# Performance work log

Hardware: AMD Instinct MI355X
Metric: run time of the kernel (lower is better)

Reference implementation:

```python
import jax, jax.numpy as jnp
import numpy as np

N_NODES = 100000


def setup_inputs() -> dict:
    key = jax.random.key(0)
    k1, k2, k3, k4, k5 = jax.random.split(key, 5)
    in_f, out_f, E = 128, 128, 1600000
    std = 1.0 / np.sqrt(out_f)
    H = jax.random.normal(k1, (N_NODES, in_f), dtype=jnp.float32)
    W = jax.random.uniform(k2, (in_f, out_f), minval=-std, maxval=std, dtype=jnp.float32)
    bias = jax.random.uniform(k3, (out_f,), minval=-std, maxval=std, dtype=jnp.float32)
    row = jax.random.randint(k4, (E,), 0, N_NODES, dtype=jnp.int32)
    col = jax.random.randint(k5, (E,), 0, N_NODES, dtype=jnp.int32)
    return {"H": H, "W": W, "bias": bias, "row": row, "col": col}


def reference(H, W, bias, row, col):
    # H: [N, in_f]; W: [in_f, out_f]; row/col: [E] edge endpoints
    Hp = jnp.matmul(H, W)  # [N, out_f]
    # edge-wise attention: leaky_relu(<Hp[i], Hp[j]>)
    scores = jax.nn.leaky_relu(jnp.sum(Hp[row] * Hp[col], axis=-1), negative_slope=0.2)  # [E]
    # scatter-softmax over rows (matches sparse_softmax: exp / (row_sum + 1e-10))
    ex = jnp.exp(scores)
    denom = jax.ops.segment_sum(ex, row, num_segments=N_NODES)  # [N]
    attn = ex / (denom[row] + 1e-10)  # [E]
    # sparse-matmul aggregation: out[i] = sum_e attn[e] * Hp[col[e]]
    out = jax.ops.segment_sum(attn[:, None] * Hp[col], row, num_segments=N_NODES)  # [N, out_f]
    return out + bias
```

## Files before the change

kernel.cpp:

```cpp
#include <hip/hip_runtime.h>
#include <hip/hip_bf16.h>

#define RSH 7
#define RPB (1 << RSH)
#define CSH 17
#define CMASK ((1 << CSH) - 1)
#define CHUNK_E 8192
#define CAP 4096
#define NBMAX 1024

typedef __attribute__((ext_vector_type(8))) _Float16 f16x8;
typedef __attribute__((ext_vector_type(2))) _Float16 f16x2;
typedef __attribute__((ext_vector_type(4))) float f32x4;

__device__ __forceinline__ unsigned int pack2h(float a, float b) {
    union { _Float16 h[2]; unsigned int u; } c;
    c.h[0] = (_Float16)a; c.h[1] = (_Float16)b;
    return c.u;
}
__device__ __forceinline__ unsigned short f2h_bits(float f) {
    union { _Float16 h; unsigned short u; } c;
    c.h = (_Float16)f;
    return c.u;
}

__global__ __launch_bounds__(256) void wsplit(
    const float* __restrict__ Wg, unsigned int* __restrict__ WhiG)
{
    int task = blockIdx.x * 256 + threadIdx.x;
    if (task >= 2048) return;
    int n  = task & 127;
    int k0 = (task >> 7) * 8;
    unsigned int hi[4];
    #pragma unroll
    for (int j = 0; j < 4; ++j) {
        float w0 = Wg[(size_t)(k0 + 2*j)     * 128 + n];
        float w1 = Wg[(size_t)(k0 + 2*j + 1) * 128 + n];
        hi[j] = pack2h(w0, w1);
    }
    int byte = (k0 * 2) ^ ((n & 7) << 4);
    *(uint4*)((char*)WhiG + n * 256 + byte) = make_uint4(hi[0], hi[1], hi[2], hi[3]);
}

__global__ __launch_bounds__(512) void gemm_hist(
    const float* __restrict__ H, const unsigned int* __restrict__ WhiG,
    unsigned short* __restrict__ Hpb, int N,
    const int* __restrict__ row, unsigned short* __restrict__ Ht,
    int E, int nchunk, int nb2, int gemmBlocks)
{
    __shared__ unsigned short Ahi[128 * 128];
    __shared__ unsigned short Whi[128 * 128];
    const int tid = threadIdx.x;

    if (blockIdx.x >= gemmBlocks) {
        int* cnt = (int*)Ahi;
        const int c = blockIdx.x - gemmBlocks;
        for (int i = tid; i < nb2; i += 512) cnt[i] = 0;
        __syncthreads();
        const int e0 = c * CHUNK_E;
        const int e1 = min(e0 + CHUNK_E, E);
        for (int e = e0 + tid; e < e1; e += 512)
            atomicAdd(&cnt[row[e] >> RSH], 1);
        __syncthreads();
        for (int i = tid; i < nb2; i += 512)
            Ht[(size_t)i * nchunk + c] = (unsigned short)cnt[i];
        return;
    }

    const int rbase = blockIdx.x * 128;

    #pragma unroll
    for (int i = 0; i < 4; ++i) {
        int idx = tid + 512 * i;
        ((uint4*)Whi)[idx] = ((const uint4*)WhiG)[idx];
    }
    #pragma unroll
    for (int i = 0; i < 8; ++i) {
        int flat = tid + 512 * i;
        int rr = flat >> 5;
        int c4  = (flat & 31) * 4;
        float4 h = make_float4(0.f, 0.f, 0.f, 0.f);
        if (rbase + rr < N)
            h = *(const float4*)&H[(size_t)(rbase + rr) * 128 + c4];
        uint2 vh;
        vh.x = pack2h(h.x, h.y);
        vh.y = pack2h(h.z, h.w);
        int byte = (c4 * 2) ^ ((rr & 7) << 4);
        *(uint2*)((char*)Ahi + rr * 256 + byte) = vh;
    }
    __syncthreads();

    const int wid = tid >> 6, lane = tid & 63;
    const int wm = wid >> 1, wn = wid & 1;
    const int lr = lane & 15, lg = lane >> 4;
    f32x4 acc[2][4] = {};

    #pragma unroll
    for (int ks = 0; ks < 4; ++ks) {
        const int kb = ks * 64 + lg * 16;
        f16x8 ahi[2];
        #pragma unroll
        for (int mi = 0; mi < 2; ++mi) {
            int rr = wm * 32 + mi * 16 + lr;
            int sw = kb ^ ((rr & 7) << 4);
            ahi[mi] = *(const f16x8*)((char*)Ahi + rr * 256 + sw);
        }
        #pragma unroll
        for (int nf = 0; nf < 4; ++nf) {
            int n = wn * 64 + nf * 16 + lr;
            int sw = kb ^ ((n & 7) << 4);
            f16x8 bhi = *(const f16x8*)((char*)Whi + n * 256 + sw);
            #pragma unroll
            for (int mi = 0; mi < 2; ++mi)
                acc[mi][nf] = __builtin_amdgcn_mfma_f32_16x16x32_f16(ahi[mi], bhi, acc[mi][nf], 0, 0, 0);
        }
    }

    #pragma unroll
    for (int mi = 0; mi < 2; ++mi) {
        #pragma unroll
        for (int nf = 0; nf < 4; ++nf) {
            int col = wn * 64 + nf * 16 + lr;
            #pragma unroll
            for (int i = 0; i < 4; ++i) {
                int rr = rbase + wm * 32 + mi * 16 + lg * 4 + i;
                if (rr < N)
                    Hpb[(size_t)rr * 128 + col] = f2h_bits(acc[mi][nf][i]);
            }
        }
    }
}

__global__ __launch_bounds__(256) void bucket_scan(
    const unsigned short* __restrict__ Ht, unsigned short* __restrict__ rel,
    int* __restrict__ totals, int nchunk)
{
    __shared__ int s[256];
    const int b = blockIdx.x, tid = threadIdx.x;
    int v = (tid < nchunk) ? (int)Ht[(size_t)b * nchunk + tid] : 0;
    s[tid] = v;
    __syncthreads();
    for (int d = 1; d < 256; d <<= 1) {
        int t = (tid >= d) ? s[tid - d] : 0;
        __syncthreads();
        s[tid] += t;
        __syncthreads();
    }
    if (tid < nchunk) rel[(size_t)b * nchunk + tid] = (unsigned short)(s[tid] - v);
    if (tid == 255) totals[b] = s[255];
}

__global__ __launch_bounds__(1024) void bucket_ptr_scan(
    const int* __restrict__ totals, int* __restrict__ bucketptr, int nb2)
{
    __shared__ int s[1024];
    const int tid = threadIdx.x;
    int v = (tid < nb2) ? totals[tid] : 0;
    s[tid] = v;
    __syncthreads();
    for (int d = 1; d < 1024; d <<= 1) {
        int t = (tid >= d) ? s[tid - d] : 0;
        __syncthreads();
        s[tid] += t;
        __syncthreads();
    }
    if (tid < nb2) bucketptr[tid] = s[tid] - v;
    if (tid == nb2 - 1) bucketptr[nb2] = s[tid];
}

__global__ __launch_bounds__(256) void chunk_scatter(
    const int* __restrict__ row, const int* __restrict__ col,
    const unsigned short* __restrict__ rel, const int* __restrict__ bucketptr,
    int* __restrict__ colsort, int E, int nchunk, int nb2)
{
    __shared__ int cur[NBMAX];
    __shared__ int gb[NBMAX];
    const int tid = threadIdx.x;
    const int c = blockIdx.x;
    const int e0 = c * CHUNK_E;
    const int tot = min(CHUNK_E, E - e0);

    for (int b = tid; b < nb2; b += 256) {
        cur[b] = 0;
        gb[b] = bucketptr[b] + (int)rel[(size_t)b * nchunk + c];
    }
    __syncthreads();

    for (int j = tid; j < tot; j += 256) {
        int r = row[e0 + j], cc = col[e0 + j];
        int b = r >> RSH;
        int p = atomicAdd(&cur[b], 1);
        colsort[gb[b] + p] = ((r & (RPB - 1)) << CSH) | cc;
    }
}

__global__ __launch_bounds__(256) void bucket_sort(
    const int* __restrict__ bucketptr, int* __restrict__ rowptr,
    int* __restrict__ colsort, int N)
{
    __shared__ int rcnt[RPB];
    __shared__ int rcur[RPB];
    __shared__ int sc[256];
    __shared__ int ord[CAP];
    const int b = blockIdx.x, tid = threadIdx.x;
    const int rbase = b << RSH;
    const int s0 = bucketptr[b];
    const int cnt = bucketptr[b + 1] - s0;

    if (tid < RPB) rcnt[tid] = 0;
    __syncthreads();
    for (int j = tid; j < cnt; j += 256)
        atomicAdd(&rcnt[colsort[s0 + j] >> CSH], 1);
    __syncthreads();

    int v = (tid < RPB) ? rcnt[tid] : 0;
    sc[tid] = v;
    __syncthreads();
    for (int d = 1; d < RPB; d <<= 1) {
        int t = (tid >= d) ? sc[tid - d] : 0;
        __syncthreads();
        sc[tid] += t;
        __syncthreads();
    }
    if (tid < RPB) {
        int ex = sc[tid] - v;
        rcur[tid] = ex;
        int r = rbase + tid;
        if (r < N) rowptr[r] = s0 + ex;
    }
    if (tid == RPB - 1) {
        int rend = min(rbase + RPB, N);
        rowptr[rend] = s0 + cnt;
    }
    __syncthreads();

    for (int j = tid; j < cnt; j += 256) {
        int rec = colsort[s0 + j];
        int p = atomicAdd(&rcur[rec >> CSH], 1);
        ord[p] = rec & CMASK;
    }
    __syncthreads();
    for (int j = tid; j < cnt; j += 256)
        colsort[s0 + j] = ord[j];
}

union F16x8U {
    uint4 v;
    f16x2 p[4];
    _Float16 h[8];
};

__device__ __forceinline__ float dot8(const f16x2* a, const F16x8U& b) {
#if __has_builtin(__builtin_amdgcn_fdot2)
    float d = __builtin_amdgcn_fdot2(a[0], b.p[0], 0.f, false);
    d = __builtin_amdgcn_fdot2(a[1], b.p[1], d, false);
    d = __builtin_amdgcn_fdot2(a[2], b.p[2], d, false);
    d = __builtin_amdgcn_fdot2(a[3], b.p[3], d, false);
    return d;
#else
    float d = 0.f;
    #pragma unroll
    for (int k = 0; k < 8; ++k)
        d = fmaf((float)a[k >> 1][k & 1], (float)b.h[k], d);
    return d;
#endif
}

__global__ __launch_bounds__(256) void aggregate_kernel(
    const unsigned short* __restrict__ Hpb, const int* __restrict__ rowptr,
    const int* __restrict__ cols, const float* __restrict__ bias,
    float* __restrict__ out, int N)
{
    const int lane = threadIdx.x & 63;
    const int wv   = threadIdx.x >> 6;
    const int r = blockIdx.x * 4 + wv;
    if (r >= N) return;
    const int d = lane & 15;
    const int g = lane >> 4;

    const float4* bp = (const float4*)&bias[d * 8];
    const float4 b0 = bp[0], b1 = bp[1];

    F16x8U hru;
    hru.v = *(const uint4*)&Hpb[(size_t)r * 128 + d * 8];
    f16x2 hr2[4] = {hru.p[0], hru.p[1], hru.p[2], hru.p[3]};

    float acc[8] = {0.f,0.f,0.f,0.f,0.f,0.f,0.f,0.f};
    float den = 0.f;
    const int e0 = rowptr[r], e1 = rowptr[r + 1];
    const int elast = e1 - 1;

    for (int e = e0 + g; e < e1; e += 8) {
        const bool m1 = (e + 4 < e1);
        const int eb = m1 ? e + 4 : elast;
        int c0 = cols[e];
        int c1 = cols[eb];
        F16x8U u0, u1;
        u0.v = *(const uint4*)&Hpb[(size_t)c0 * 128 + d * 8];
        u1.v = *(const uint4*)&Hpb[(size_t)c1 * 128 + d * 8];

        float dot0 = dot8(hr2, u0);
        float dot1 = dot8(hr2, u1);

        dot0 += __shfl_xor(dot0, 1);
        dot1 += __shfl_xor(dot1, 1);
        dot0 += __shfl_xor(dot0, 2);
        dot1 += __shfl_xor(dot1, 2);
        dot0 += __shfl_xor(dot0, 4);
        dot1 += __shfl_xor(dot1, 4);
        dot0 += __shfl_xor(dot0, 8);
        dot1 += __shfl_xor(dot1, 8);

        float s0 = fmaxf(dot0, 0.2f * dot0);
        float s1 = fmaxf(dot1, 0.2f * dot1);
        float ex0 = __expf(s0);
        float ex1 = m1 ? __expf(s1) : 0.f;
        den += ex0 + ex1;
        #pragma unroll
        for (int k = 0; k < 8; ++k) {
            acc[k] = fmaf((float)u0.h[k], ex0, acc[k]);
            acc[k] = fmaf((float)u1.h[k], ex1, acc[k]);
        }
    }

    #pragma unroll
    for (int k = 0; k < 8; ++k) {
        acc[k] += __shfl_xor(acc[k], 16);
        acc[k] += __shfl_xor(acc[k], 32);
    }
    den += __shfl_xor(den, 16);
    den += __shfl_xor(den, 32);

    if (g == 0) {
        float inv = 1.f / (den + 1e-10f);
        float4 o0, o1;
        o0.x = fmaf(acc[0], inv, b0.x);
        o0.y = fmaf(acc[1], inv, b0.y);
        o0.z = fmaf(acc[2], inv, b0.z);
        o0.w = fmaf(acc[3], inv, b0.w);
        o1.x = fmaf(acc[4], inv, b1.x);
        o1.y = fmaf(acc[5], inv, b1.y);
        o1.z = fmaf(acc[6], inv, b1.z);
        o1.w = fmaf(acc[7], inv, b1.w);
        float4* op = (float4*)&out[(size_t)r * 128 + d * 8];
        op[0] = o0;
        op[1] = o1;
    }
}

extern "C" void kernel_launch(void* const* d_in, const int* in_sizes, int n_in,
                              void* d_out, int out_size, void* d_ws, size_t ws_size,
                              hipStream_t stream)
{
    const float* H    = (const float*)d_in[0];
    const float* W    = (const float*)d_in[1];
    const float* bias = (const float*)d_in[2];
    const int*   row  = (const int*)d_in[3];
    const int*   col  = (const int*)d_in[4];
    const int N = in_sizes[0] / 128;
    const int E = in_sizes[3];

    const int nchunk = (E + CHUNK_E - 1) / CHUNK_E;
    const int nb2    = (N + RPB - 1) / RPB;

    auto align = [](size_t x) { return (x + 255) & ~(size_t)255; };

    char* ws = (char*)d_ws;
    size_t off = 0;
    unsigned short* Hpb       = (unsigned short*)(ws + off); off = align(off + (size_t)N * 128 * 2);
    unsigned short* Ht        = (unsigned short*)(ws + off); off = align(off + (size_t)nb2 * nchunk * 2);
    unsigned short* rel       = (unsigned short*)(ws + off); off = align(off + (size_t)nb2 * nchunk * 2);
    int*            totals    = (int*)(ws + off);            off = align(off + (size_t)nb2 * 4);
    int*            bucketptr = (int*)(ws + off);            off = align(off + (size_t)(nb2 + 1) * 4);
    int*            rowptr    = (int*)(ws + off);            off = align(off + (size_t)(N + 1) * 4);
    unsigned int*   WhiG      = (unsigned int*)(ws + off);   off = align(off + 8192 * 4);
    int*            colsort   = (int*)(ws + off);

    const int gemmBlocks = (N + 127) / 128;

    wsplit<<<8, 256, 0, stream>>>(W, WhiG);
    gemm_hist<<<gemmBlocks + nchunk, 512, 0, stream>>>(H, WhiG, Hpb, N,
                                                       row, Ht, E, nchunk, nb2,
                                                       gemmBlocks);
    bucket_scan<<<nb2, 256, 0, stream>>>(Ht, rel, totals, nchunk);
    bucket_ptr_scan<<<1, 1024, 0, stream>>>(totals, bucketptr, nb2);
    chunk_scatter<<<nchunk, 256, 0, stream>>>(row, col, rel, bucketptr,
                                              colsort, E, nchunk, nb2);
    bucket_sort<<<nb2, 256, 0, stream>>>(bucketptr, rowptr, colsort, N);
    aggregate_kernel<<<(N + 3) / 4, 256, 0, stream>>>(Hpb, rowptr, colsort, bias,
                                                      (float*)d_out, N);
}
```

Before: 123.3 us.

## Fuse per-bucket row sort into aggregation kernel using shared-memory edge list

```diff
diff --git a/kernel.cpp b/kernel.cpp
--- a/kernel.cpp
+++ b/kernel.cpp
@@ -194,56 +194,6 @@
     }
 }
 
-__global__ __launch_bounds__(256) void bucket_sort(
-    const int* __restrict__ bucketptr, int* __restrict__ rowptr,
-    int* __restrict__ colsort, int N)
-{
-    __shared__ int rcnt[RPB];
-    __shared__ int rcur[RPB];
-    __shared__ int sc[256];
-    __shared__ int ord[CAP];
-    const int b = blockIdx.x, tid = threadIdx.x;
-    const int rbase = b << RSH;
-    const int s0 = bucketptr[b];
-    const int cnt = bucketptr[b + 1] - s0;
-
-    if (tid < RPB) rcnt[tid] = 0;
-    __syncthreads();
-    for (int j = tid; j < cnt; j += 256)
-        atomicAdd(&rcnt[colsort[s0 + j] >> CSH], 1);
-    __syncthreads();
-
-    int v = (tid < RPB) ? rcnt[tid] : 0;
-    sc[tid] = v;
-    __syncthreads();
-    for (int d = 1; d < RPB; d <<= 1) {
-        int t = (tid >= d) ? sc[tid - d] : 0;
-        __syncthreads();
-        sc[tid] += t;
-        __syncthreads();
-    }
-    if (tid < RPB) {
-        int ex = sc[tid] - v;
-        rcur[tid] = ex;
-        int r = rbase + tid;
-        if (r < N) rowptr[r] = s0 + ex;
-    }
-    if (tid == RPB - 1) {
-        int rend = min(rbase + RPB, N);
-        rowptr[rend] = s0 + cnt;
-    }
-    __syncthreads();
-
-    for (int j = tid; j < cnt; j += 256) {
-        int rec = colsort[s0 + j];
-        int p = atomicAdd(&rcur[rec >> CSH], 1);
-        ord[p] = rec & CMASK;
-    }
-    __syncthreads();
-    for (int j = tid; j < cnt; j += 256)
-        colsort[s0 + j] = ord[j];
-}
-
 union F16x8U {
     uint4 v;
     f16x2 p[4];
@@ -266,72 +216,104 @@
 #endif
 }
 
-__global__ __launch_bounds__(256) void aggregate_kernel(
-    const unsigned short* __restrict__ Hpb, const int* __restrict__ rowptr,
-    const int* __restrict__ cols, const float* __restrict__ bias,
+__global__ __launch_bounds__(512) void bucket_aggregate(
+    const unsigned short* __restrict__ Hpb, const int* __restrict__ bucketptr,
+    const int* __restrict__ colsort, const float* __restrict__ bias,
     float* __restrict__ out, int N)
 {
-    const int lane = threadIdx.x & 63;
-    const int wv   = threadIdx.x >> 6;
-    const int r = blockIdx.x * 4 + wv;
-    if (r >= N) return;
+    __shared__ int ord[CAP];
+    __shared__ int rowoff[RPB + 1];
+    __shared__ int rcur[RPB];
+    __shared__ int sc[RPB];
+    const int b = blockIdx.x, tid = threadIdx.x;
+    const int rbase = b << RSH;
+    const int s0 = bucketptr[b];
+    const int cnt = bucketptr[b + 1] - s0;
+
+    if (tid < RPB) rcur[tid] = 0;
+    __syncthreads();
+    for (int j = tid; j < cnt; j += 512)
+        atomicAdd(&rcur[colsort[s0 + j] >> CSH], 1);
+    __syncthreads();
+
+    int v = (tid < RPB) ? rcur[tid] : 0;
+    if (tid < RPB) sc[tid] = v;
+    __syncthreads();
+    for (int dd = 1; dd < RPB; dd <<= 1) {
+        int t = (tid >= dd && tid < RPB) ? sc[tid - dd] : 0;
+        __syncthreads();
+        if (tid < RPB) sc[tid] += t;
+        __syncthreads();
+    }
+    if (tid < RPB) {
+        int ex = sc[tid] - v;
+        rowoff[tid] = ex;
+        rcur[tid] = ex;
+    }
+    if (tid == 0) rowoff[RPB] = cnt;
+    __syncthreads();
+
+    for (int j = tid; j < cnt; j += 512) {
+        int rec = colsort[s0 + j];
+        int p = atomicAdd(&rcur[rec >> CSH], 1);
+        ord[p] = rec & CMASK;
+    }
+    __syncthreads();
+
+    const int lane = tid & 63;
+    const int wv = tid >> 6;
+    const int g = lane >> 4;
     const int d = lane & 15;
-    const int g = lane >> 4;
+    const int gi = wv * 4 + g;
 
     const float4* bp = (const float4*)&bias[d * 8];
     const float4 b0 = bp[0], b1 = bp[1];
 
-    F16x8U hru;
-    hru.v = *(const uint4*)&Hpb[(size_t)r * 128 + d * 8];
-    f16x2 hr2[4] = {hru.p[0], hru.p[1], hru.p[2], hru.p[3]};
-
-    float acc[8] = {0.f,0.f,0.f,0.f,0.f,0.f,0.f,0.f};
-    float den = 0.f;
-    const int e0 = rowptr[r], e1 = rowptr[r + 1];
-    const int elast = e1 - 1;
-
-    for (int e = e0 + g; e < e1; e += 8) {
-        const bool m1 = (e + 4 < e1);
-        const int eb = m1 ? e + 4 : elast;
-        int c0 = cols[e];
-        int c1 = cols[eb];
-        F16x8U u0, u1;
-        u0.v = *(const uint4*)&Hpb[(size_t)c0 * 128 + d * 8];
-        u1.v = *(const uint4*)&Hpb[(size_t)c1 * 128 + d * 8];
-
-        float dot0 = dot8(hr2, u0);
-        float dot1 = dot8(hr2, u1);
-
-        dot0 += __shfl_xor(dot0, 1);
-        dot1 += __shfl_xor(dot1, 1);
-        dot0 += __shfl_xor(dot0, 2);
-        dot1 += __shfl_xor(dot1, 2);
-        dot0 += __shfl_xor(dot0, 4);
-        dot1 += __shfl_xor(dot1, 4);
-        dot0 += __shfl_xor(dot0, 8);
-        dot1 += __shfl_xor(dot1, 8);
-
-        float s0 = fmaxf(dot0, 0.2f * dot0);
-        float s1 = fmaxf(dot1, 0.2f * dot1);
-        float ex0 = __expf(s0);
-        float ex1 = m1 ? __expf(s1) : 0.f;
-        den += ex0 + ex1;
-        #pragma unroll
-        for (int k = 0; k < 8; ++k) {
-            acc[k] = fmaf((float)u0.h[k], ex0, acc[k]);
-            acc[k] = fmaf((float)u1.h[k], ex1, acc[k]);
+    for (int lr = gi; lr < RPB; lr += 32) {
+        const int r = rbase + lr;
+        if (r >= N) continue;
+
+        F16x8U hru;
+        hru.v = *(const uint4*)&Hpb[(size_t)r * 128 + d * 8];
+        f16x2 hr2[4] = {hru.p[0], hru.p[1], hru.p[2], hru.p[3]};
+
+        float acc[8] = {0.f,0.f,0.f,0.f,0.f,0.f,0.f,0.f};
+        float den = 0.f;
+        const int e0 = rowoff[lr], e1 = rowoff[lr + 1];
+        const int elast = e1 - 1;
+
+        for (int e = e0; e < e1; e += 2) {
+            const bool m1 = (e + 1 < e1);
+            int c0 = ord[e];
+            int c1 = ord[m1 ? e + 1 : elast];
+            F16x8U u0, u1;
+            u0.v = *(const uint4*)&Hpb[(size_t)c0 * 128 + d * 8];
+            u1.v = *(const uint4*)&Hpb[(size_t)c1 * 128 + d * 8];
+
+            float dot0 = dot8(hr2, u0);
+            float dot1 = dot8(hr2, u1);
+
+            dot0 += __shfl_xor(dot0, 1);
+            dot1 += __shfl_xor(dot1, 1);
+            dot0 += __shfl_xor(dot0, 2);
+            dot1 += __shfl_xor(dot1, 2);
+            dot0 += __shfl_xor(dot0, 4);
+            dot1 += __shfl_xor(dot1, 4);
+            dot0 += __shfl_xor(dot0, 8);
+            dot1 += __shfl_xor(dot1, 8);
+
+            float s0f = fmaxf(dot0, 0.2f * dot0);
+            float s1f = fmaxf(dot1, 0.2f * dot1);
+            float ex0 = __expf(s0f);
+            float ex1 = m1 ? __expf(s1f) : 0.f;
+            den += ex0 + ex1;
+            #pragma unroll
+            for (int k = 0; k < 8; ++k) {
+                acc[k] = fmaf((float)u0.h[k], ex0, acc[k]);
+                acc[k] = fmaf((float)u1.h[k], ex1, acc[k]);
+            }
         }
-    }
-
-    #pragma unroll
-    for (int k = 0; k < 8; ++k) {
-        acc[k] += __shfl_xor(acc[k], 16);
-        acc[k] += __shfl_xor(acc[k], 32);
-    }
-    den += __shfl_xor(den, 16);
-    den += __shfl_xor(den, 32);
-
-    if (g == 0) {
+
         float inv = 1.f / (den + 1e-10f);
         float4 o0, o1;
         o0.x = fmaf(acc[0], inv, b0.x);
@@ -372,7 +354,6 @@
     unsigned short* rel       = (unsigned short*)(ws + off); off = align(off + (size_t)nb2 * nchunk * 2);
     int*            totals    = (int*)(ws + off);            off = align(off + (size_t)nb2 * 4);
     int*            bucketptr = (int*)(ws + off);            off = align(off + (size_t)(nb2 + 1) * 4);
-    int*            rowptr    = (int*)(ws + off);            off = align(off + (size_t)(N + 1) * 4);
     unsigned int*   WhiG      = (unsigned int*)(ws + off);   off = align(off + 8192 * 4);
     int*            colsort   = (int*)(ws + off);
 
@@ -386,7 +367,6 @@
     bucket_ptr_scan<<<1, 1024, 0, stream>>>(totals, bucketptr, nb2);
     chunk_scatter<<<nchunk, 256, 0, stream>>>(row, col, rel, bucketptr,
                                               colsort, E, nchunk, nb2);
-    bucket_sort<<<nb2, 256, 0, stream>>>(bucketptr, rowptr, colsort, N);
-    aggregate_kernel<<<(N + 3) / 4, 256, 0, stream>>>(Hpb, rowptr, colsort, bias,
-                                                      (float*)d_out, N);
-}
+    bucket_aggregate<<<nb2, 512, 0, stream>>>(Hpb, bucketptr, colsort, bias,
+                                              (float*)d_out, N);
+}
```

Measured after the change: 137.0 us. +11.1%, slower.
